# Performance work log

Measured on AMD Instinct MI355X. Metric: run time of the kernel, lower is better.

## Reference

```python
import jax, jax.numpy as jnp
import numpy as np


def _gat(x, adj, W, a):
    # x: [N, J, Fin], W: [H, Fin, hs], a: [H, 2*hs]
    # e_ij = leakyrelu(a1.Wh_i + a2.Wh_j)  (decomposed form of the repeat/cat construction)
    hs = W.shape[-1]
    Wh = jnp.einsum('bjf,hfd->bhjd', x, W)
    s1 = jnp.einsum('bhjd,hd->bhj', Wh, a[:, :hs])
    s2 = jnp.einsum('bhjd,hd->bhj', Wh, a[:, hs:])
    e = jax.nn.leaky_relu(s1[..., :, None] + s2[..., None, :], 0.2)
    e = jnp.where(adj[None, None] > 0, e, jnp.float32(-9e15))
    att = jax.nn.softmax(e, axis=-1)
    h = jnp.einsum('bhij,bhjd->bhid', att, Wh)
    b, H, j, d = h.shape
    return jax.nn.elu(h.transpose(0, 2, 1, 3).reshape(b, j, H * d))


def _conv_bn_relu(x, w, bias, g, be, m, v):
    # x: [N, C, T], w: [O, I, 3], BN in inference mode
    y = jax.lax.conv_general_dilated(x, w, (1,), [(1, 1)], dimension_numbers=('NCH', 'OIH', 'NCH'))
    y = y + bias[None, :, None]
    y = (y - m[None, :, None]) / jnp.sqrt(v[None, :, None] + 1e-5) * g[None, :, None] + be[None, :, None]
    return jax.nn.relu(y)


def _mha(q, k, v, wq, bq, wk, bk, wv, bv, wo, bo):
    # torch nn.MultiheadAttention, 4 heads, eval mode (no dropout)
    n, L, D = q.shape
    H = 4
    hd = D // H
    def proj(x, w, b):
        return (x @ w.T + b).reshape(n, -1, H, hd)
    Q, K, V = proj(q, wq, bq), proj(k, wk, bk), proj(v, wv, bv)
    att = jax.nn.softmax(jnp.einsum('nqhd,nkhd->nhqk', Q, K) * jnp.float32(1.0 / np.sqrt(hd)), axis=-1)
    o = jnp.einsum('nhqk,nkhd->nqhd', att, V).reshape(n, L, D)
    return o @ wo.T + bo


def _lstm_dir(x, wih, whh, bih, bhh, rev):
    # x: [B, T, D]; torch gate order i, f, g, o
    b, t, _ = x.shape
    H = whh.shape[1]
    xw = jnp.transpose(x @ wih.T + (bih + bhh), (1, 0, 2))  # [T, B, 4H]
    def step(carry, xt):
        h, c = carry
        gates = xt + h @ whh.T
        i, f, g, o = jnp.split(gates, 4, axis=-1)
        c = jax.nn.sigmoid(f) * c + jax.nn.sigmoid(i) * jnp.tanh(g)
        h = jax.nn.sigmoid(o) * jnp.tanh(c)
        return (h, c), h
    init = (jnp.zeros((b, H), x.dtype), jnp.zeros((b, H), x.dtype))
    _, hs = jax.lax.scan(step, init, xw, reverse=rev)
    return jnp.transpose(hs, (1, 0, 2))


def _forward(lh, rh, adj, vis, g1W, g1a, g2W, g2a, c1w, c1b, b1g, b1b, b1m, b1v, c2w, c2b, b2g, b2b, b2m, b2v,
             wq, bq, wk, bk, wv, bv, wo, bo,
             l0fw, l0fu, l0fbi, l0fbh, l0bw, l0bu, l0bbi, l0bbh,
             l1fw, l1fu, l1fbi, l1fbh, l1bw, l1bu, l1bbi, l1bbh,
             o1w, o1b, o2w, o2b):
    B, T, J, F = lh.shape

    def single_hand(x):
        h = x.reshape(B * T, J, F)
        h = _gat(h, adj, g1W, g1a)
        h = _gat(h, adj, g2W, g2a)
        D = h.shape[-1]
        ht = h.reshape(B, T, J, D).transpose(0, 2, 3, 1).reshape(B * J, D, T)
        ht = _conv_bn_relu(ht, c1w, c1b, b1g, b1b, b1m, b1v)
        ht = _conv_bn_relu(ht, c2w, c2b, b2g, b2b, b2m, b2v)
        return ht.reshape(B, J, D, T).transpose(0, 3, 1, 2)  # [B, T, J, D]

    l = single_hand(lh)
    r = single_hand(rh)
    D = l.shape[-1]
    lf = l.reshape(B * T, J, D)
    rf = r.reshape(B * T, J, D)
    a_l2r = _mha(lf, rf, rf, wq, bq, wk, bk, wv, bv, wo, bo)
    a_r2l = _mha(rf, lf, lf, wq, bq, wk, bk, wv, bv, wo, bo)
    # repair of shape-inconsistent torch reshape: pool joints before the seq LSTM
    le = (lf + 0.5 * a_r2l).reshape(B, T, J, D).mean(axis=2)
    re = (rf + 0.5 * a_l2r).reshape(B, T, J, D).mean(axis=2)

    def bilstm(x):
        h1 = jnp.concatenate([_lstm_dir(x, l0fw, l0fu, l0fbi, l0fbh, False),
                              _lstm_dir(x, l0bw, l0bu, l0bbi, l0bbh, True)], -1)
        return jnp.concatenate([_lstm_dir(h1, l1fw, l1fu, l1fbi, l1fbh, False),
                                _lstm_dir(h1, l1bw, l1bu, l1bbi, l1bbh, True)], -1)

    def head(x):
        y = jax.nn.relu(x @ o1w.T + o1b) @ o2w.T + o2b  # [B, T, 3*J]
        return y.reshape(B, T, J, 3)

    lp = head(bilstm(le)) * vis[..., None]
    rp = head(bilstm(re)) * vis[..., None]
    return lp, rp


def setup_inputs() -> dict:
    key = jax.random.key(0)
    ks = jax.random.split(key, 60)
    it = iter(range(60))
    B, T, J, F, D = 8, 512, 21, 512, 256
    def nrm(shape, s=0.05):
        return jax.random.normal(ks[next(it)], shape, jnp.float32) * s
    inp = {}
    inp['left_hand_feats'] = nrm((B, T, J, F), 1.0)
    inp['right_hand_feats'] = nrm((B, T, J, F), 1.0)
    adj = (jax.random.uniform(ks[next(it)], (J, J)) < 0.3).astype(jnp.float32)
    inp['hand_adj_matrix'] = jnp.maximum(adj, jnp.eye(J, dtype=jnp.float32))
    inp['hand_visibility'] = jax.random.uniform(ks[next(it)], (B, T, J), jnp.float32)
    inp['gat1_W'] = nrm((4, F, 64)); inp['gat1_a'] = nrm((4, 128))
    inp['gat2_W'] = nrm((4, D, 64)); inp['gat2_a'] = nrm((4, 128))
    inp['conv1_w'] = nrm((D, D, 3)); inp['conv1_b'] = nrm((D,))
    inp['conv2_w'] = nrm((D, D, 3)); inp['conv2_b'] = nrm((D,))
    for p in ['bn1', 'bn2']:
        inp[p + '_g'] = jnp.ones((D,), jnp.float32)
        inp[p + '_b'] = jnp.zeros((D,), jnp.float32)
        inp[p + '_m'] = jnp.zeros((D,), jnp.float32)
        inp[p + '_v'] = jnp.ones((D,), jnp.float32)
    for p in ['attn_wq', 'attn_wk', 'attn_wv', 'attn_wo']:
        inp[p] = nrm((D, D))
    for p in ['attn_bq', 'attn_bk', 'attn_bv', 'attn_bo']:
        inp[p] = nrm((D,))
    H = D // 2
    for l in ['lstm0f', 'lstm0b', 'lstm1f', 'lstm1b']:
        inp[l + '_wih'] = nrm((4 * H, D))
        inp[l + '_whh'] = nrm((4 * H, H))
        inp[l + '_bih'] = nrm((4 * H,))
        inp[l + '_bhh'] = nrm((4 * H,))
    inp['out1_w'] = nrm((D, D)); inp['out1_b'] = nrm((D,))
    inp['out2_w'] = nrm((3 * J, D)); inp['out2_b'] = nrm((3 * J,))
    return inp


def reference(left_hand_feats, right_hand_feats, hand_adj_matrix, hand_visibility,
              gat1_W, gat1_a, gat2_W, gat2_a,
              conv1_w, conv1_b, bn1_g, bn1_b, bn1_m, bn1_v,
              conv2_w, conv2_b, bn2_g, bn2_b, bn2_m, bn2_v,
              attn_wq, attn_bq, attn_wk, attn_bk, attn_wv, attn_bv, attn_wo, attn_bo,
              lstm0f_wih, lstm0f_whh, lstm0f_bih, lstm0f_bhh,
              lstm0b_wih, lstm0b_whh, lstm0b_bih, lstm0b_bhh,
              lstm1f_wih, lstm1f_whh, lstm1f_bih, lstm1f_bhh,
              lstm1b_wih, lstm1b_whh, lstm1b_bih, lstm1b_bhh,
              out1_w, out1_b, out2_w, out2_b):
    return _forward(left_hand_feats, right_hand_feats, hand_adj_matrix, hand_visibility,
                    gat1_W, gat1_a, gat2_W, gat2_a,
                    conv1_w, conv1_b, bn1_g, bn1_b, bn1_m, bn1_v,
                    conv2_w, conv2_b, bn2_g, bn2_b, bn2_m, bn2_v,
                    attn_wq, attn_bq, attn_wk, attn_bk, attn_wv, attn_bv, attn_wo, attn_bo,
                    lstm0f_wih, lstm0f_whh, lstm0f_bih, lstm0f_bhh,
                    lstm0b_wih, lstm0b_whh, lstm0b_bih, lstm0b_bhh,
                    lstm1f_wih, lstm1f_whh, lstm1f_bih, lstm1f_bhh,
                    lstm1b_wih, lstm1b_whh, lstm1b_bih, lstm1b_bhh,
                    out1_w, out1_b, out2_w, out2_b)
```

## Files before the change

kernel.cpp:

```cpp
#include <hip/hip_runtime.h>

typedef __bf16 bf16;
typedef bf16 bf16x8 __attribute__((ext_vector_type(8)));
typedef float f32x4 __attribute__((ext_vector_type(4)));
typedef _Float16 f16;
typedef f16 f16x8 __attribute__((ext_vector_type(8)));

#define NBT 4096
#define NJ 21
#define NLF 86016
#define DD 256
#define CONVM1 86352
#define CONVM2 172704
#define SPAD 514
#define CROWS_ALL 173056

__device__ __forceinline__ void gload16(const bf16* g, bf16* l) {
  __builtin_amdgcn_global_load_lds(
      (const __attribute__((address_space(1))) unsigned int*)g,
      (__attribute__((address_space(3))) unsigned int*)l, 16, 0, 0);
}

__global__ __launch_bounds__(256, 2) void gemm_bf16(
    const void* __restrict__ Av, const bf16* __restrict__ Bt,
    float* __restrict__ C32, bf16* __restrict__ Cout,
    const float* __restrict__ bias, const float* __restrict__ sc,
    const float* __restrict__ sh, int M, int N, int K, int lda, int flags)
{
  __shared__ __align__(16) bf16 As[2][128][32];
  __shared__ __align__(16) bf16 Bs[2][128][32];
  const int tid = threadIdx.x;
  const long m0 = (long)blockIdx.y * 128;
  const int n0 = blockIdx.x * 128;
  const int wave = tid >> 6, lane = tid & 63;
  const int wm = (wave & 1) * 64, wn = (wave >> 1) * 64;
  const int frow = lane & 15, fkb = (lane >> 4) * 8;
  const int crow = lane >> 2, ccol = (lane & 3) * 8;
  const bf16* Ab = (const bf16*)Av;
  const float* Af = (const float*)Av;
  const int nk = K >> 5;
  const int ch0 = wave * 2, ch1 = ch0 + 1;
  const long arow0 = (m0 + ch0 * 16 + crow) * (long)lda + ccol;
  const long arow1 = (m0 + ch1 * 16 + crow) * (long)lda + ccol;
  const long brow0 = ((long)(n0 + ch0 * 16 + crow)) * K + ccol;
  const long brow1 = ((long)(n0 + ch1 * 16 + crow)) * K + ccol;
  const int lr = tid >> 1, lc = (tid & 1) * 16;

  auto stageA_f32 = [&](int buf, int k0) {
    const float* ap = Af + (m0 + lr) * (long)lda + (k0 + lc);
    bf16x8 t0, t1;
    #pragma unroll
    for (int u = 0; u < 8; u++) { t0[u] = (bf16)ap[u]; t1[u] = (bf16)ap[8 + u]; }
    *(bf16x8*)(&As[buf][lr][lc])     = t0;
    *(bf16x8*)(&As[buf][lr][lc + 8]) = t1;
  };

  f32x4 acc[4][4] = {};
  if (flags & 1) stageA_f32(0, 0);
  else {
    gload16(Ab + arow0, &As[0][ch0 * 16][0]);
    gload16(Ab + arow1, &As[0][ch1 * 16][0]);
  }
  gload16(Bt + brow0, &Bs[0][ch0 * 16][0]);
  gload16(Bt + brow1, &Bs[0][ch1 * 16][0]);

  for (int kt = 0; kt < nk; kt++) {
    const int cur = kt & 1;
    if (kt + 1 < nk) {
      const int k0 = (kt + 1) << 5;
      if (flags & 1) {
        stageA_f32(cur ^ 1, k0);
        gload16(Bt + brow0 + k0, &Bs[cur ^ 1][ch0 * 16][0]);
        gload16(Bt + brow1 + k0, &Bs[cur ^ 1][ch1 * 16][0]);
        asm volatile("s_waitcnt vmcnt(2) lgkmcnt(0)" ::: "memory");
      } else {
        gload16(Ab + arow0 + k0, &As[cur ^ 1][ch0 * 16][0]);
        gload16(Ab + arow1 + k0, &As[cur ^ 1][ch1 * 16][0]);
        gload16(Bt + brow0 + k0, &Bs[cur ^ 1][ch0 * 16][0]);
        gload16(Bt + brow1 + k0, &Bs[cur ^ 1][ch1 * 16][0]);
        asm volatile("s_waitcnt vmcnt(4) lgkmcnt(0)" ::: "memory");
      }
    } else {
      asm volatile("s_waitcnt vmcnt(0) lgkmcnt(0)" ::: "memory");
    }
    __builtin_amdgcn_sched_barrier(0);
    __builtin_amdgcn_s_barrier();
    __builtin_amdgcn_sched_barrier(0);
    bf16x8 af[4], bg[4];
    #pragma unroll
    for (int i = 0; i < 4; i++) af[i] = *(const bf16x8*)(&As[cur][wm + i * 16 + frow][fkb]);
    #pragma unroll
    for (int j = 0; j < 4; j++) bg[j] = *(const bf16x8*)(&Bs[cur][wn + j * 16 + frow][fkb]);
    #pragma unroll
    for (int i = 0; i < 4; i++)
      #pragma unroll
      for (int j = 0; j < 4; j++)
        acc[i][j] = __builtin_amdgcn_mfma_f32_16x16x32_bf16(af[i], bg[j], acc[i][j], 0, 0, 0);
    asm volatile("s_waitcnt lgkmcnt(0)" ::: "memory");
    __builtin_amdgcn_sched_barrier(0);
    __builtin_amdgcn_s_barrier();
    __builtin_amdgcn_sched_barrier(0);
  }
  const int col = lane & 15, rbase = (lane >> 4) * 4;
  #pragma unroll
  for (int i = 0; i < 4; i++) {
    #pragma unroll
    for (int j = 0; j < 4; j++) {
      const int nn = n0 + wn + j * 16 + col;
      #pragma unroll
      for (int r = 0; r < 4; r++) {
        const long mm = m0 + wm + i * 16 + rbase + r;
        if (mm >= M) continue;
        float v = acc[i][j][r];
        if (flags & 2) { C32[mm * (long)N + nn] = v; continue; }
        if (flags & 8) v = v * sc[nn] + sh[nn];
        else if (bias) v += bias[nn];
        if (flags & 4) v = fmaxf(v, 0.f);
        if (flags & 16) {
          const int s = (int)(mm % SPAD);
          if (s == 0 || s == SPAD - 1) v = 0.f;
          Cout[mm * (long)N + nn] = (bf16)v;
        } else if (flags & 32) {
          const long hj = mm / SPAD; const int s = (int)(mm - hj * SPAD);
          if (s == 0 || s == SPAD - 1) continue;
          const int hand = (int)(hj / 168); const int lhj = (int)(hj - hand * 168);
          const int b = lhj / NJ; const int j2 = lhj - b * NJ;
          const long dst = (long)hand * NLF + ((long)b * 512 + (s - 1)) * NJ + j2;
          Cout[dst * (long)N + nn] = (bf16)v;
        } else {
          Cout[mm * (long)N + nn] = (bf16)v;
        }
      }
    }
  }
}

__global__ void cvt_k(const float* __restrict__ s, bf16* __restrict__ d, long n) {
  long i = (long)blockIdx.x * 256 + threadIdx.x;
  if (i < n) d[i] = (bf16)s[i];
}
__global__ void prep_gatW(const float* __restrict__ W, bf16* __restrict__ Wt, int F) {
  long idx = (long)blockIdx.x * 256 + threadIdx.x;
  if (idx >= 256L * F) return;
  int n = (int)(idx / F), f = (int)(idx % F);
  Wt[idx] = (bf16)W[((long)(n >> 6) * F + f) * 64 + (n & 63)];
}
__global__ void prep_convw(const float* __restrict__ w, bf16* __restrict__ wp) {
  int idx = blockIdx.x * 256 + threadIdx.x;
  int n = idx / 768, k = idx % 768, tap = k >> 8, i = k & 255;
  wp[idx] = (bf16)w[(n * 256 + i) * 3 + tap];
}
__global__ void prep_out2(const float* __restrict__ w, bf16* __restrict__ wp) {
  int idx = blockIdx.x * 256 + threadIdx.x;
  wp[idx] = (idx < 63 * 256) ? (bf16)w[idx] : (bf16)0.f;
}
__global__ void prep_scsh(const float* __restrict__ cb, const float* __restrict__ g,
                          const float* __restrict__ be, const float* __restrict__ m,
                          const float* __restrict__ v, float* __restrict__ sc,
                          float* __restrict__ sh) {
  int c = threadIdx.x;
  float rs = rsqrtf(v[c] + 1e-5f) * g[c];
  sc[c] = rs; sh[c] = (cb[c] - m[c]) * rs + be[c];
}
__global__ void prep_bkv(const float* __restrict__ bk, const float* __restrict__ bv,
                         float* __restrict__ o) {
  int i = blockIdx.x * 256 + threadIdx.x;
  if (i >= 512) return;
  o[i] = (i < 256) ? bk[i] : bv[i - 256];
}
__global__ void pad_zero(bf16* __restrict__ convIn) {
  int idx = blockIdx.x * 256 + threadIdx.x;
  int hj = idx >> 9, s = ((idx >> 8) & 1) ? (SPAD - 1) : 0, c = idx & 255;
  convIn[((long)hj * SPAD + s) * DD + c] = (bf16)0.f;
}
__global__ void zero_out(float* __restrict__ o, long n) {
  long i = (long)blockIdx.x * 256 + threadIdx.x;
  if (i < n) o[i] = 0.f;
}

__global__ __launch_bounds__(256) void gat_attn(
    const bf16* __restrict__ Wh, const float* __restrict__ a,
    const float* __restrict__ adj, bf16* __restrict__ out, int convMode)
{
  const int bt = blockIdx.x, tid = threadIdx.x;
  __shared__ float whs[NJ][DD];
  __shared__ float s1[4][NJ], s2[4][NJ];
  __shared__ float att[4][NJ][NJ];
  const long base = (long)bt * NJ * DD;
  for (int i = tid; i < NJ * DD; i += 256)
    whs[i >> 8][i & 255] = (float)Wh[base + i];
  __syncthreads();
  if (tid < 4 * NJ) {
    const int h = tid / NJ, i = tid % NJ;
    float x1 = 0.f, x2 = 0.f;
    for (int d = 0; d < 64; d++) {
      const float w = whs[i][h * 64 + d];
      x1 += w * a[h * 128 + d];
      x2 += w * a[h * 128 + 64 + d];
    }
    s1[h][i] = x1; s2[h][i] = x2;
  }
  __syncthreads();
  for (int idx = tid; idx < 4 * NJ * NJ; idx += 256) {
    const int h = idx / (NJ * NJ), r = idx % (NJ * NJ), i = r / NJ, j = r % NJ;
    float e = s1[h][i] + s2[h][j];
    e = e > 0.f ? e : 0.2f * e;
    att[h][i][j] = (adj[i * NJ + j] > 0.f) ? e : -9e15f;
  }
  __syncthreads();
  if (tid < 4 * NJ) {
    const int h = tid / NJ, i = tid % NJ;
    float mx = -3e38f;
    for (int j = 0; j < NJ; j++) mx = fmaxf(mx, att[h][i][j]);
    float sum = 0.f;
    for (int j = 0; j < NJ; j++) { const float ex = __expf(att[h][i][j] - mx); att[h][i][j] = ex; sum += ex; }
    const float inv = 1.f / sum;
    for (int j = 0; j < NJ; j++) att[h][i][j] *= inv;
  }
  __syncthreads();
  const int hand = bt >> 12, b = (bt >> 9) & 7, t = bt & 511;
  for (int idx = tid; idx < NJ * DD; idx += 256) {
    const int i = idx >> 8, c = idx & 255, h = c >> 6;
    float s = 0.f;
    for (int j = 0; j < NJ; j++) s += att[h][i][j] * whs[j][c];
    s = s > 0.f ? s : (__expf(s) - 1.f);
    const long row = convMode
        ? ((long)hand * CONVM1 + ((long)(b * NJ + i)) * SPAD + (t + 1))
        : ((long)bt * NJ + i);
    out[row * DD + c] = (bf16)s;
  }
}

__global__ __launch_bounds__(256) void mha_core2(
    const bf16* __restrict__ Q, const bf16* __restrict__ KV,
    bf16* __restrict__ O)
{
  const int bt = blockIdx.x, tid = threadIdx.x;
  __shared__ bf16 qs[NJ][DD], ks[NJ][DD], vs[NJ][DD];
  __shared__ float att[4][NJ][NJ];
  const long baseq = (long)bt * NJ * DD;
  const long basekv = (long)bt * NJ * 512;
  for (int i = tid; i < NJ * DD; i += 256) {
    const int r = i >> 8, c = i & 255;
    qs[r][c] = Q[baseq + i];
    ks[r][c] = KV[basekv + r * 512 + c];
    vs[r][c] = KV[basekv + r * 512 + 256 + c];
  }
  __syncthreads();
  for (int idx = tid; idx < 4 * NJ * NJ; idx += 256) {
    const int h = idx / (NJ * NJ), r = idx % (NJ * NJ), i = r / NJ, j = r % NJ;
    float s = 0.f;
    for (int d = 0; d < 64; d++) s += (float)qs[i][h * 64 + d] * (float)ks[j][h * 64 + d];
    att[h][i][j] = s * 0.125f;
  }
  __syncthreads();
  if (tid < 4 * NJ) {
    const int h = tid / NJ, i = tid % NJ;
    float mx = -3e38f;
    for (int j = 0; j < NJ; j++) mx = fmaxf(mx, att[h][i][j]);
    float sum = 0.f;
    for (int j = 0; j < NJ; j++) { const float ex = __expf(att[h][i][j] - mx); att[h][i][j] = ex; sum += ex; }
    const float inv = 1.f / sum;
    for (int j = 0; j < NJ; j++) att[h][i][j] *= inv;
  }
  __syncthreads();
  for (int idx = tid; idx < NJ * DD; idx += 256) {
    const int i = idx >> 8, c = idx & 255, h = c >> 6;
    float s = 0.f;
    for (int j = 0; j < NJ; j++) s += att[h][i][j] * (float)vs[j][c];
    O[baseq + i * DD + c] = (bf16)s;
  }
}

__global__ __launch_bounds__(256) void pool_kernel(
    const bf16* __restrict__ lf, const bf16* __restrict__ ao, bf16* __restrict__ o)
{
  const int bt = blockIdx.x, c = threadIdx.x;
  float s = 0.f;
  for (int j = 0; j < NJ; j++) {
    const long r = ((long)bt * NJ + j) * DD + c;
    s += (float)lf[r] + 0.5f * (float)ao[r];
  }
  o[(long)bt * DD + c] = (bf16)(s * (1.f / 21.f));
}

#define REP16(X) X(0) X(1) X(2) X(3) X(4) X(5) X(6) X(7) X(8) X(9) X(10) X(11) \
  X(12) X(13) X(14) X(15)

#define LDS_FENCE() do { \
  asm volatile("s_waitcnt lgkmcnt(0)" ::: "memory"); \
  __builtin_amdgcn_sched_barrier(0); \
  __builtin_amdgcn_s_barrier(); \
  __builtin_amdgcn_sched_barrier(0); \
} while (0)

__global__ __launch_bounds__(512, 1) void lstm_lds(
    const float* __restrict__ xw,
    const float* __restrict__ whhF, const float* __restrict__ whhB,
    const float* __restrict__ bihF, const float* __restrict__ bhhF,
    const float* __restrict__ bihB, const float* __restrict__ bhhB,
    bf16* __restrict__ outL, bf16* __restrict__ outR)
{
  const int wg = blockIdx.x;
  const int hand = wg >> 4, dir = (wg >> 3) & 1, b = wg & 7;
  const int tid = threadIdx.x;
  const float* whh = dir ? whhB : whhF;

  __shared__ f16 whhs[512][136];
  __shared__ f16 hbuf[136];
  __shared__ float gsb[512];

  for (int i = tid; i < 512 * 128; i += 512)
    whhs[i >> 7][i & 127] = (f16)whh[i];
  if (tid < 136) hbuf[tid] = (f16)0.f;
  const float bias = (dir ? bihB : bihF)[tid] + (dir ? bhhB : bhhF)[tid];
  float c = 0.f;
  const float* xp = xw + ((long)hand * NBT + (long)b * 512) * 1024 + dir * 512;
  bf16* outp = hand ? outR : outL;
  float xv = xp[(long)(dir ? 511 : 0) * 1024 + tid];
  __syncthreads();

  const f16* wrow = &whhs[tid][0];
#define WRD(i) f16x8 w##i = *(const f16x8*)(wrow + (i) * 8);
  REP16(WRD)
#undef WRD

  for (int s = 0; s < 512; s++) {
    const int t = dir ? (511 - s) : s;
    const int tn = dir ? (510 - s) : (s + 1);
    float xnext = 0.f;
    if (s < 511) xnext = xp[(long)tn * 1024 + tid];
    float a0 = xv + bias, a1 = 0.f, a2 = 0.f, a3 = 0.f;
#define WDOT(i) { \
    const f16x8 hv = *(const f16x8*)(&hbuf[(i) * 8]); \
    a0 = __builtin_amdgcn_fdot2(__builtin_shufflevector(w##i, w##i, 0, 1), \
                                __builtin_shufflevector(hv, hv, 0, 1), a0, false); \
    a1 = __builtin_amdgcn_fdot2(__builtin_shufflevector(w##i, w##i, 2, 3), \
                                __builtin_shufflevector(hv, hv, 2, 3), a1, false); \
    a2 = __builtin_amdgcn_fdot2(__builtin_shufflevector(w##i, w##i, 4, 5), \
                                __builtin_shufflevector(hv, hv, 4, 5), a2, false); \
    a3 = __builtin_amdgcn_fdot2(__builtin_shufflevector(w##i, w##i, 6, 7), \
                                __builtin_shufflevector(hv, hv, 6, 7), a3, false); }
    REP16(WDOT)
#undef WDOT
    gsb[tid] = (a0 + a1) + (a2 + a3);
    LDS_FENCE();
    if (tid < 128) {
      const float ig = gsb[tid], fg = gsb[tid + 128], gg = gsb[tid + 256], og = gsb[tid + 384];
      const float si = __builtin_amdgcn_rcpf(1.f + __expf(-ig));
      const float sf = __builtin_amdgcn_rcpf(1.f + __expf(-fg));
      const float so = __builtin_amdgcn_rcpf(1.f + __expf(-og));
      const float tg = 1.f - 2.f * __builtin_amdgcn_rcpf(1.f + __expf(2.f * gg));
      c = sf * c + si * tg;
      const float tc = 1.f - 2.f * __builtin_amdgcn_rcpf(1.f + __expf(2.f * c));
      const float h = so * tc;
      hbuf[tid] = (f16)h;
      outp[((long)b * 512 + t) * 256 + dir * 128 + tid] = (bf16)h;
    }
    LDS_FENCE();
    xv = xnext;
  }
}

__global__ __launch_bounds__(256) void finalize_k(
    const float* __restrict__ y, const float* __restrict__ b2,
    const float* __restrict__ vis, float* __restrict__ out)
{
  const int idx = blockIdx.x * 256 + threadIdx.x;
  if (idx >= 2 * NBT * 63) return;
  const int c = idx % 63; const int r = idx / 63; const int bt = r & (NBT - 1);
  out[idx] = (y[(long)r * 128 + c] + b2[c]) * vis[bt * 21 + (c / 3)];
}

extern "C" void kernel_launch(void* const* d_in, const int* in_sizes, int n_in,
                              void* d_out, int out_size, void* d_ws, size_t ws_size,
                              hipStream_t stream) {
  (void)in_sizes; (void)n_in;
  const float* feats[2] = { (const float*)d_in[0], (const float*)d_in[1] };
  const float* adj  = (const float*)d_in[2];
  const float* vis  = (const float*)d_in[3];
  const float* gW[2] = { (const float*)d_in[4], (const float*)d_in[6] };
  const float* ga[2] = { (const float*)d_in[5], (const float*)d_in[7] };
  const float* cw_[2] = { (const float*)d_in[8],  (const float*)d_in[10] };
  const float* cb_[2] = { (const float*)d_in[9],  (const float*)d_in[11] };
  const float* bng[2] = { (const float*)d_in[12], (const float*)d_in[16] };
  const float* bnb[2] = { (const float*)d_in[13], (const float*)d_in[17] };
  const float* bnm[2] = { (const float*)d_in[14], (const float*)d_in[18] };
  const float* bnv[2] = { (const float*)d_in[15], (const float*)d_in[19] };
  const float* wq = (const float*)d_in[20], *wk = (const float*)d_in[21];
  const float* wv = (const float*)d_in[22], *wo = (const float*)d_in[23];
  const float* bq = (const float*)d_in[24], *bk = (const float*)d_in[25];
  const float* bv = (const float*)d_in[26], *bo = (const float*)d_in[27];
  const float* Lwih[2][2] = { { (const float*)d_in[28], (const float*)d_in[32] },
                              { (const float*)d_in[36], (const float*)d_in[40] } };
  const float* Lwhh[2][2] = { { (const float*)d_in[29], (const float*)d_in[33] },
                              { (const float*)d_in[37], (const float*)d_in[41] } };
  const float* Lbih[2][2] = { { (const float*)d_in[30], (const float*)d_in[34] },
                              { (const float*)d_in[38], (const float*)d_in[42] } };
  const float* Lbhh[2][2] = { { (const float*)d_in[31], (const float*)d_in[35] },
                              { (const float*)d_in[39], (const float*)d_in[43] } };
  const float* o1w = (const float*)d_in[44], *o1b = (const float*)d_in[45];
  const float* o2w = (const float*)d_in[46], *o2b = (const float*)d_in[47];

  char* base = (char*)d_ws;
  size_t off = 0;
  auto alloc = [&](size_t b) { size_t r = off; off += (b + 1023) & ~(size_t)1023; return r; };
  const size_t SZ_BIG = (size_t)CROWS_ALL * DD * 2;
  const size_t SZ_BT  = (size_t)NBT * DD * 2;
  const size_t o_w1t = alloc((size_t)256 * 512 * 2);
  const size_t o_w2t = alloc((size_t)256 * 256 * 2);
  const size_t o_cw1 = alloc((size_t)256 * 768 * 2);
  const size_t o_cw2 = alloc((size_t)256 * 768 * 2);
  const size_t o_wq  = alloc((size_t)256 * 256 * 2);
  const size_t o_wk  = alloc((size_t)256 * 256 * 2);
  const size_t o_wv  = alloc((size_t)256 * 256 * 2);
  const size_t o_wo  = alloc((size_t)256 * 256 * 2);
  const size_t o_o1w = alloc((size_t)256 * 256 * 2);
  const size_t o_o2p = alloc((size_t)128 * 256 * 2);
  const size_t o_lw0 = alloc((size_t)512 * 256 * 2);
  const size_t o_lw1 = alloc((size_t)512 * 256 * 2);
  const size_t o_lw2 = alloc((size_t)512 * 256 * 2);
  const size_t o_lw3 = alloc((size_t)512 * 256 * 2);
  const size_t o_ss  = alloc((size_t)4 * 256 * 4);
  const size_t o_bkv = alloc((size_t)512 * 4);
  const size_t o_BA  = alloc(SZ_BIG);
  const size_t o_BH  = alloc(SZ_BIG);
  const size_t o_lfL = alloc((size_t)NLF * DD * 2);
  const size_t o_lfR = alloc((size_t)NLF * DD * 2);
  const size_t o_le  = alloc(SZ_BT);
  const size_t o_re  = alloc(SZ_BT);
  const size_t o_h1L = alloc(SZ_BT);
  const size_t o_h1R = alloc(SZ_BT);
  const size_t o_hoL = alloc(SZ_BT);
  const size_t o_hoR = alloc(SZ_BT);
  const size_t NEED = off;
  if (ws_size < NEED) {
    zero_out<<<(out_size + 255) / 256, 256, 0, stream>>>((float*)d_out, out_size);
    return;
  }
  auto P = [&](size_t o_) { return (void*)(base + o_); };

  auto gemm = [&](const void* A, const void* Bt, void* c32, void* co,
                  const void* bias_, const void* sc_, const void* sh_,
                  long M, int N, int K, int lda, int flags) {
    dim3 g((unsigned)(N / 128), (unsigned)((M + 127) / 128));
    gemm_bf16<<<g, 256, 0, stream>>>(A, (const bf16*)Bt, (float*)c32, (bf16*)co,
                                     (const float*)bias_, (const float*)sc_,
                                     (const float*)sh_, (int)M, N, K, lda, flags);
  };
  auto cvt = [&](const float* s, void* d, long n) {
    cvt_k<<<(unsigned)((n + 255) / 256), 256, 0, stream>>>(s, (bf16*)d, n);
  };

  prep_gatW<<<512, 256, 0, stream>>>(gW[0], (bf16*)P(o_w1t), 512);
  prep_gatW<<<256, 256, 0, stream>>>(gW[1], (bf16*)P(o_w2t), 256);
  prep_convw<<<768, 256, 0, stream>>>(cw_[0], (bf16*)P(o_cw1));
  prep_convw<<<768, 256, 0, stream>>>(cw_[1], (bf16*)P(o_cw2));
  cvt(wq, P(o_wq), 65536); cvt(wk, P(o_wk), 65536);
  cvt(wv, P(o_wv), 65536); cvt(wo, P(o_wo), 65536);
  cvt(o1w, P(o_o1w), 65536);
  cvt(Lwih[0][0], P(o_lw0), 131072); cvt(Lwih[0][1], P(o_lw1), 131072);
  cvt(Lwih[1][0], P(o_lw2), 131072); cvt(Lwih[1][1], P(o_lw3), 131072);
  prep_out2<<<128, 256, 0, stream>>>(o2w, (bf16*)P(o_o2p));
  float* sc1 = (float*)P(o_ss); float* sh1 = sc1 + 256;
  float* sc2 = sh1 + 256;       float* sh2 = sc2 + 256;
  prep_scsh<<<1, 256, 0, stream>>>(cb_[0], bng[0], bnb[0], bnm[0], bnv[0], sc1, sh1);
  prep_scsh<<<1, 256, 0, stream>>>(cb_[1], bng[1], bnb[1], bnm[1], bnv[1], sc2, sh2);
  prep_bkv<<<2, 256, 0, stream>>>(bk, bv, (float*)P(o_bkv));

  bf16* BA = (bf16*)P(o_BA);
  bf16* BH = (bf16*)P(o_BH);
  bf16* lfb[2] = { (bf16*)P(o_lfL), (bf16*)P(o_lfR) };

  for (int hd = 0; hd < 2; hd++)
    gemm(feats[hd], P(o_w1t), nullptr, BA + (size_t)hd * NLF * DD,
         nullptr, nullptr, nullptr, NLF, 256, 512, 512, 1);
  gat_attn<<<2 * NBT, 256, 0, stream>>>(BA, ga[0], adj, BA, 0);
  gemm(BA, P(o_w2t), nullptr, BH, nullptr, nullptr, nullptr,
       2 * NLF, 256, 256, 256, 0);
  pad_zero<<<672, 256, 0, stream>>>(BA + DD);
  gat_attn<<<2 * NBT, 256, 0, stream>>>(BH, ga[1], adj, BA + DD, 1);
  gemm(BA, P(o_cw1), nullptr, BH + DD, nullptr, sc1, sh1,
       CONVM2, 256, 768, 256, 8 | 4 | 16);
  gemm(BH, P(o_cw2), nullptr, lfb[0], nullptr, sc2, sh2,
       CONVM2, 256, 768, 256, 8 | 4 | 32);

  bf16* Bwo = BA + (size_t)NLF * DD;
  for (int pass = 0; pass < 2; pass++) {
    const bf16* qsrc = lfb[pass];
    const bf16* kvsrc = lfb[1 - pass];
    gemm(kvsrc, P(o_wk), nullptr, BH, P(o_bkv), nullptr, nullptr,
         NLF, 512, 256, 256, 0);
    gemm(qsrc, P(o_wq), nullptr, BA, bq, nullptr, nullptr, NLF, 256, 256, 256, 0);
    mha_core2<<<NBT, 256, 0, stream>>>(BA, BH, BA);
    gemm(BA, P(o_wo), nullptr, Bwo, bo, nullptr, nullptr, NLF, 256, 256, 256, 0);
    pool_kernel<<<NBT, 256, 0, stream>>>(kvsrc, Bwo,
        (bf16*)P(pass == 0 ? o_re : o_le));
  }

  float* xw = (float*)P(o_BH);
  gemm(P(o_le), P(o_lw0), xw, nullptr, nullptr, nullptr, nullptr,
       2 * NBT, 1024, 256, 256, 2);
  lstm_lds<<<32, 512, 0, stream>>>(xw, Lwhh[0][0], Lwhh[0][1],
      Lbih[0][0], Lbhh[0][0], Lbih[0][1], Lbhh[0][1],
      (bf16*)P(o_h1L), (bf16*)P(o_h1R));
  gemm(P(o_h1L), P(o_lw2), xw, nullptr, nullptr, nullptr, nullptr,
       2 * NBT, 1024, 256, 256, 2);
  lstm_lds<<<32, 512, 0, stream>>>(xw, Lwhh[1][0], Lwhh[1][1],
      Lbih[1][0], Lbhh[1][0], Lbih[1][1], Lbhh[1][1],
      (bf16*)P(o_hoL), (bf16*)P(o_hoR));

  gemm(P(o_hoL), P(o_o1w), nullptr, BA, o1b, nullptr, nullptr,
       2 * NBT, 256, 256, 256, 4);
  float* y32 = (float*)P(o_BH);
  gemm(BA, P(o_o2p), y32, nullptr, nullptr, nullptr, nullptr,
       2 * NBT, 128, 256, 256, 2);
  finalize_k<<<(2 * NBT * 63 + 255) / 256, 256, 0, stream>>>(
      y32, o2b, vis, (float*)d_out);
}
```

Measured before the change: 2.129 ms.

## Batch cross-attention passes, fuse finalize into GEMM epilogue, move gate activations

The two cross-hand attention passes now share batched Q and output-projection GEMMs over both hands, and a single pool kernel covers both passes, which cuts the number of kernel launches. The final bias-and-visibility step moves into the last GEMM's epilogue through a new flag, removing the separate finalize kernel and the fp32 round trip it needed. In the LSTM, all 512 threads now apply their own gate's sigmoid or tanh before the barrier, instead of 128 threads computing four activations each, which shortens the serial part of every step. The batched layout relies on the left and right buffers being contiguous and on the BH scratch space being large enough.

```diff
diff --git a/kernel.cpp b/kernel.cpp
--- a/kernel.cpp
+++ b/kernel.cpp
@@ -112,6 +112,13 @@
         const long mm = m0 + wm + i * 16 + rbase + r;
         if (mm >= M) continue;
         float v = acc[i][j][r];
+        if (flags & 64) {
+          if (nn < 63) {
+            float vv = (v + bias[nn]) * sc[(mm & (NBT - 1)) * 21 + nn / 3];
+            C32[mm * 63 + nn] = vv;
+          }
+          continue;
+        }
         if (flags & 2) { C32[mm * (long)N + nn] = v; continue; }
         if (flags & 8) v = v * sc[nn] + sh[nn];
         else if (bias) v += bias[nn];
@@ -272,16 +279,18 @@
   }
 }
 
-__global__ __launch_bounds__(256) void pool_kernel(
-    const bf16* __restrict__ lf, const bf16* __restrict__ ao, bf16* __restrict__ o)
+__global__ __launch_bounds__(256) void pool2_kernel(
+    const bf16* __restrict__ lfBase, const bf16* __restrict__ ao,
+    bf16* __restrict__ leBase)
 {
-  const int bt = blockIdx.x, c = threadIdx.x;
+  const int b = blockIdx.x, c = threadIdx.x;
+  const int h = b >> 12, bt = b & (NBT - 1);
+  const bf16* lfp = lfBase + ((long)(1 - h) * NLF + (long)bt * NJ) * DD;
+  const bf16* aop = ao + ((long)b * NJ) * DD;
   float s = 0.f;
-  for (int j = 0; j < NJ; j++) {
-    const long r = ((long)bt * NJ + j) * DD + c;
-    s += (float)lf[r] + 0.5f * (float)ao[r];
-  }
-  o[(long)bt * DD + c] = (bf16)(s * (1.f / 21.f));
+  for (int j = 0; j < NJ; j++)
+    s += (float)lfp[j * DD + c] + 0.5f * (float)aop[j * DD + c];
+  leBase[((long)(1 - h) * NBT + bt) * DD + c] = (bf16)(s * (1.f / 21.f));
 }
 
 #define REP16(X) X(0) X(1) X(2) X(3) X(4) X(5) X(6) X(7) X(8) X(9) X(10) X(11) \
@@ -317,6 +326,7 @@
   float c = 0.f;
   const float* xp = xw + ((long)hand * NBT + (long)b * 512) * 1024 + dir * 512;
   bf16* outp = hand ? outR : outL;
+  const bool isG = (tid >> 7) == 2;
   float xv = xp[(long)(dir ? 511 : 0) * 1024 + tid];
   __syncthreads();
 
@@ -343,14 +353,15 @@
                                 __builtin_shufflevector(hv, hv, 6, 7), a3, false); }
     REP16(WDOT)
 #undef WDOT
-    gsb[tid] = (a0 + a1) + (a2 + a3);
+    {
+      const float g = (a0 + a1) + (a2 + a3);
+      gsb[tid] = isG ? (1.f - 2.f * __builtin_amdgcn_rcpf(1.f + __expf(2.f * g)))
+                     : __builtin_amdgcn_rcpf(1.f + __expf(-g));
+    }
     LDS_FENCE();
     if (tid < 128) {
-      const float ig = gsb[tid], fg = gsb[tid + 128], gg = gsb[tid + 256], og = gsb[tid + 384];
-      const float si = __builtin_amdgcn_rcpf(1.f + __expf(-ig));
-      const float sf = __builtin_amdgcn_rcpf(1.f + __expf(-fg));
-      const float so = __builtin_amdgcn_rcpf(1.f + __expf(-og));
-      const float tg = 1.f - 2.f * __builtin_amdgcn_rcpf(1.f + __expf(2.f * gg));
+      const float si = gsb[tid],       sf = gsb[tid + 128];
+      const float tg = gsb[tid + 256], so = gsb[tid + 384];
       c = sf * c + si * tg;
       const float tc = 1.f - 2.f * __builtin_amdgcn_rcpf(1.f + __expf(2.f * c));
       const float h = so * tc;
@@ -360,16 +371,6 @@
     LDS_FENCE();
     xv = xnext;
   }
-}
-
-__global__ __launch_bounds__(256) void finalize_k(
-    const float* __restrict__ y, const float* __restrict__ b2,
-    const float* __restrict__ vis, float* __restrict__ out)
-{
-  const int idx = blockIdx.x * 256 + threadIdx.x;
-  if (idx >= 2 * NBT * 63) return;
-  const int c = idx % 63; const int r = idx / 63; const int bt = r & (NBT - 1);
-  out[idx] = (y[(long)r * 128 + c] + b2[c]) * vis[bt * 21 + (c / 3)];
 }
 
 extern "C" void kernel_launch(void* const* d_in, const int* in_sizes, int n_in,
@@ -485,18 +486,13 @@
   gemm(BH, P(o_cw2), nullptr, lfb[0], nullptr, sc2, sh2,
        CONVM2, 256, 768, 256, 8 | 4 | 32);
 
-  bf16* Bwo = BA + (size_t)NLF * DD;
-  for (int pass = 0; pass < 2; pass++) {
-    const bf16* qsrc = lfb[pass];
-    const bf16* kvsrc = lfb[1 - pass];
-    gemm(kvsrc, P(o_wk), nullptr, BH, P(o_bkv), nullptr, nullptr,
-         NLF, 512, 256, 256, 0);
-    gemm(qsrc, P(o_wq), nullptr, BA, bq, nullptr, nullptr, NLF, 256, 256, 256, 0);
-    mha_core2<<<NBT, 256, 0, stream>>>(BA, BH, BA);
-    gemm(BA, P(o_wo), nullptr, Bwo, bo, nullptr, nullptr, NLF, 256, 256, 256, 0);
-    pool_kernel<<<NBT, 256, 0, stream>>>(kvsrc, Bwo,
-        (bf16*)P(pass == 0 ? o_re : o_le));
-  }
+  gemm(lfb[0], P(o_wq), nullptr, BA, bq, nullptr, nullptr, 2 * NLF, 256, 256, 256, 0);
+  gemm(lfb[1], P(o_wk), nullptr, BH, P(o_bkv), nullptr, nullptr, NLF, 512, 256, 256, 0);
+  mha_core2<<<NBT, 256, 0, stream>>>(BA, BH, BA);
+  gemm(lfb[0], P(o_wk), nullptr, BH, P(o_bkv), nullptr, nullptr, NLF, 512, 256, 256, 0);
+  mha_core2<<<NBT, 256, 0, stream>>>(BA + (size_t)NLF * DD, BH, BA + (size_t)NLF * DD);
+  gemm(BA, P(o_wo), nullptr, BH, bo, nullptr, nullptr, 2 * NLF, 256, 256, 256, 0);
+  pool2_kernel<<<2 * NBT, 256, 0, stream>>>(lfb[0], BH, (bf16*)P(o_le));
 
   float* xw = (float*)P(o_BH);
   gemm(P(o_le), P(o_lw0), xw, nullptr, nullptr, nullptr, nullptr,
@@ -512,9 +508,6 @@
 
   gemm(P(o_hoL), P(o_o1w), nullptr, BA, o1b, nullptr, nullptr,
        2 * NBT, 256, 256, 256, 4);
-  float* y32 = (float*)P(o_BH);
-  gemm(BA, P(o_o2p), y32, nullptr, nullptr, nullptr, nullptr,
-       2 * NBT, 128, 256, 256, 2);
-  finalize_k<<<(2 * NBT * 63 + 255) / 256, 256, 0, stream>>>(
-      y32, o2b, vis, (float*)d_out);
-}
+  gemm(BA, P(o_o2p), d_out, nullptr, o2b, vis, nullptr,
+       2 * NBT, 128, 256, 256, 64);
+}
```

Result: no change. 2.110 ms (median of 2 runs) (-0.9%).
